# Optimization experiments

Measured on AMD Instinct MI355X. Metric: run time of the kernel, lower is better.

The kernel has to match this reference:

```python
import jax, jax.numpy as jnp
import numpy as np

DIM = 1024
NUM_HEADS = 16
HEAD_DIM = DIM // NUM_HEADS


def setup_inputs() -> dict:
    key = jax.random.key(0)
    ks = jax.random.split(key, 9)
    B, T, D = 4, 8192, DIM
    s = 1.0 / np.sqrt(D)
    return {
        "x": jax.random.normal(ks[0], (B, T, D), dtype=jnp.float32),
        "Wq": jax.random.normal(ks[1], (D, D), dtype=jnp.float32) * s,
        "bq": jnp.zeros((D,), dtype=jnp.float32),
        "Wk": jax.random.normal(ks[2], (D, D), dtype=jnp.float32) * s,
        "bk": jnp.zeros((D,), dtype=jnp.float32),
        "Wv": jax.random.normal(ks[3], (D, D), dtype=jnp.float32) * s,
        "bv": jnp.zeros((D,), dtype=jnp.float32),
        "Wo": jax.random.normal(ks[4], (D, D), dtype=jnp.float32) * s,
        "bo": jnp.zeros((D,), dtype=jnp.float32),
    }


def _feature_map(x):
    # elu(x) + 1
    return jax.nn.elu(x) + 1.0


def reference(x, Wq, bq, Wk, bk, Wv, bv, Wo, bo):
    B, T, D = x.shape
    H, hd = NUM_HEADS, HEAD_DIM
    q = (x @ Wq.T + bq).reshape(B, T, H, hd)
    k = (x @ Wk.T + bk).reshape(B, T, H, hd)
    v = (x @ Wv.T + bv).reshape(B, T, H, hd)
    q = _feature_map(q)
    k = _feature_map(k)
    eps = 1e-6
    kv = jnp.einsum('bthd,bthm->bhmd', k, v)      # [B,H,hd,hd]
    k_sum = k.sum(axis=1)                          # [B,H,hd]
    z = 1.0 / (jnp.einsum('bthd,bhd->bth', q, k_sum) + eps)
    out = jnp.einsum('bthd,bhmd->bthm', q, kv) * z[..., None]
    out = out.reshape(B, T, D)
    return out @ Wo.T + bo
```

## Files before the change

### kernel.cpp

```cpp
#include <hip/hip_runtime.h>
#include <stdint.h>

typedef __bf16 bf16x8 __attribute__((ext_vector_type(8)));
typedef float f32x4 __attribute__((ext_vector_type(4)));
typedef unsigned short u16x8 __attribute__((ext_vector_type(8)));
typedef unsigned short u16x4 __attribute__((ext_vector_type(4)));

#define MFMA16(a, b, c) __builtin_amdgcn_mfma_f32_16x16x32_bf16(a, b, c, 0, 0, 0)
#define BAR() __builtin_amdgcn_s_barrier()
#define LGK0() do { asm volatile("s_waitcnt lgkmcnt(0)" ::: "memory"); \
                    __builtin_amdgcn_sched_barrier(0); } while (0)
#define VMC(n) asm volatile("s_waitcnt vmcnt(" #n ")" ::: "memory")
#define PRIO(p) __builtin_amdgcn_s_setprio(p)

#define TSEQ 8192
#define BATCH 4

static __device__ __forceinline__ unsigned short f2bf(float f) {
  union { float f; unsigned u; } v; v.f = f;
  unsigned u = v.u + 0x7FFFu + ((v.u >> 16) & 1u);
  return (unsigned short)(u >> 16);
}
static __device__ __forceinline__ float bf2f(unsigned short h) {
  union { unsigned u; float f; } v; v.u = ((unsigned)h) << 16; return v.f;
}
static __device__ __forceinline__ void gload16(const void* g, void* l) {
  __builtin_amdgcn_global_load_lds((const __attribute__((address_space(1))) void*)g,
                                   (__attribute__((address_space(3))) void*)l, 16, 0, 0);
}

__global__ __launch_bounds__(256) void cvt_bf16(const float* __restrict__ s,
                                                unsigned short* __restrict__ d, int n) {
  int i = (blockIdx.x * 256 + threadIdx.x) * 8;
  if (i >= n) return;
  const float4 a = *(const float4*)(s + i);
  const float4 b = *(const float4*)(s + i + 4);
  u16x8 o;
  o[0] = f2bf(a.x); o[1] = f2bf(a.y); o[2] = f2bf(a.z); o[3] = f2bf(a.w);
  o[4] = f2bf(b.x); o[5] = f2bf(b.y); o[6] = f2bf(b.z); o[7] = f2bf(b.w);
  *(u16x8*)(d + i) = o;
}


static __device__ __forceinline__ void stage_ht(const unsigned short* __restrict__ G,
                                                int grow0, char* Lbase, int t, int h,
                                                int tid, int w) {
  const int prow = tid >> 2, cp = tid & 3;
  const int gch = cp ^ ((prow >> 1) & 3);
  const unsigned short* src = G + (size_t)(grow0 + h * 128 + prow) * 1024 + t * 32 + gch * 8;
  char* dst = Lbase + (t & 1) * 16384 + h * 8192 + w * 1024;
  gload16(src, dst);
}

static __device__ __forceinline__ void mfma_quad(f32x4 acc[8][4], const bf16x8* a,
                                                 const bf16x8* b, int m0) {
  #pragma unroll
  for (int mf = 0; mf < 4; ++mf)
    #pragma unroll
    for (int nf = 0; nf < 4; ++nf)
      acc[m0 + mf][nf] = MFMA16(a[m0 + mf], b[nf], acc[m0 + mf][nf]);
}

static __device__ __forceinline__ void gemm256(const unsigned short* __restrict__ A,
                                               const unsigned short* __restrict__ B,
                                               int rowA0, int rowB0,
                                               char* As, char* Bs, f32x4 acc[8][4]) {
  const int tid = threadIdx.x, l = tid & 63, w = tid >> 6;
  const int wr = w >> 2, wc = w & 3;
  int a_off[8], b_off[4];
  #pragma unroll
  for (int mf = 0; mf < 8; ++mf) {
    const int r = wr * 128 + mf * 16 + (l & 15);
    const int cp = (l >> 4) ^ ((r >> 1) & 3);
    a_off[mf] = r * 64 + cp * 16;
  }
  #pragma unroll
  for (int nf = 0; nf < 4; ++nf) {
    const int r = wc * 64 + nf * 16 + (l & 15);
    const int cp = (l >> 4) ^ ((r >> 1) & 3);
    b_off[nf] = r * 64 + cp * 16;
  }
  stage_ht(A, rowA0, As, 0, 0, tid, w);
  stage_ht(A, rowA0, As, 0, 1, tid, w);
  stage_ht(B, rowB0, Bs, 0, 0, tid, w);
  stage_ht(B, rowB0, Bs, 0, 1, tid, w);
  stage_ht(A, rowA0, As, 1, 0, tid, w);
  stage_ht(A, rowA0, As, 1, 1, tid, w);
  VMC(2);
  BAR();

  #pragma unroll 1
  for (int i = 0; i < 15; ++i) {
    const int t1 = 2 * i + 1;
    bf16x8 a0[8], b0[4];
    #pragma unroll
    for (int mf = 0; mf < 8; ++mf) a0[mf] = *(const bf16x8*)(As + a_off[mf]);
    #pragma unroll
    for (int nf = 0; nf < 4; ++nf) b0[nf] = *(const bf16x8*)(Bs + b_off[nf]);
    stage_ht(B, rowB0, Bs, t1, 0, tid, w);
    stage_ht(B, rowB0, Bs, t1, 1, tid, w);
    BAR(); LGK0(); PRIO(1);
    mfma_quad(acc, a0, b0, 0);
    PRIO(0); BAR();
    stage_ht(A, rowA0, As, t1 + 1, 0, tid, w);
    stage_ht(A, rowA0, As, t1 + 1, 1, tid, w);
    BAR(); PRIO(1);
    mfma_quad(acc, a0, b0, 4);
    PRIO(0);
    VMC(2);
    BAR();
    bf16x8 a1[8], b1[4];
    #pragma unroll
    for (int mf = 0; mf < 8; ++mf) a1[mf] = *(const bf16x8*)(As + 16384 + a_off[mf]);
    #pragma unroll
    for (int nf = 0; nf < 4; ++nf) b1[nf] = *(const bf16x8*)(Bs + 16384 + b_off[nf]);
    stage_ht(B, rowB0, Bs, t1 + 1, 0, tid, w);
    stage_ht(B, rowB0, Bs, t1 + 1, 1, tid, w);
    BAR(); LGK0(); PRIO(1);
    mfma_quad(acc, a1, b1, 0);
    PRIO(0); BAR();
    stage_ht(A, rowA0, As, t1 + 2, 0, tid, w);
    stage_ht(A, rowA0, As, t1 + 2, 1, tid, w);
    BAR(); PRIO(1);
    mfma_quad(acc, a1, b1, 4);
    PRIO(0);
    VMC(2);
    BAR();
  }
  {
    bf16x8 a0[8], b0[4];
    #pragma unroll
    for (int mf = 0; mf < 8; ++mf) a0[mf] = *(const bf16x8*)(As + a_off[mf]);
    #pragma unroll
    for (int nf = 0; nf < 4; ++nf) b0[nf] = *(const bf16x8*)(Bs + b_off[nf]);
    stage_ht(B, rowB0, Bs, 31, 0, tid, w);
    stage_ht(B, rowB0, Bs, 31, 1, tid, w);
    BAR(); LGK0(); PRIO(1);
    mfma_quad(acc, a0, b0, 0);
    PRIO(0); BAR();
    PRIO(1);
    mfma_quad(acc, a0, b0, 4);
    PRIO(0);
    VMC(0);
    BAR();
    bf16x8 a1[8], b1[4];
    #pragma unroll
    for (int mf = 0; mf < 8; ++mf) a1[mf] = *(const bf16x8*)(As + 16384 + a_off[mf]);
    #pragma unroll
    for (int nf = 0; nf < 4; ++nf) b1[nf] = *(const bf16x8*)(Bs + 16384 + b_off[nf]);
    LGK0(); PRIO(1);
    mfma_quad(acc, a1, b1, 0);
    mfma_quad(acc, a1, b1, 4);
    PRIO(0);
  }
}

__global__ __launch_bounds__(512, 2) void qkv_gemm256(
    const unsigned short* __restrict__ xbf, const unsigned short* __restrict__ wcat,
    const float* __restrict__ bq, const float* __restrict__ bk, const float* __restrict__ bv,
    unsigned short* __restrict__ qout, unsigned short* __restrict__ kout,
    unsigned short* __restrict__ vout) {
  __shared__ char As[32768];
  __shared__ char Bs[32768];
  const int swz = (blockIdx.x & 7) * 192 + (blockIdx.x >> 3);
  const int mt = swz / 12, nt = swz % 12;
  f32x4 acc[8][4] = {};
  gemm256(xbf, wcat, mt * 256, nt * 256, As, Bs, acc);

  const int l = threadIdx.x & 63, w = threadIdx.x >> 6;
  const int wr = w >> 2, wc = w & 3;
  const int region = nt >> 2;
  const float* bias = (region == 0) ? bq : (region == 1) ? bk : bv;
  unsigned short* dst = (region == 0) ? qout : (region == 1) ? kout : vout;
  const int colb = (nt & 3) * 256 + wc * 64;
  #pragma unroll
  for (int mf = 0; mf < 8; ++mf) {
    #pragma unroll
    for (int nf = 0; nf < 4; ++nf) {
      const int col = colb + nf * 16 + (l & 15);
      const float bb = bias[col];
      #pragma unroll
      for (int j = 0; j < 4; ++j) {
        const int row = mt * 256 + wr * 128 + mf * 16 + (l >> 4) * 4 + j;
        float v = acc[mf][nf][j] + bb;
        if (region < 2) v = (v > 0.f) ? (v + 1.f) : __expf(v);
        dst[(size_t)row * 1024 + col] = f2bf(v);
      }
    }
  }
}

__global__ __launch_bounds__(512, 2) void o_gemm256(
    const unsigned short* __restrict__ attn, const unsigned short* __restrict__ wo,
    const float* __restrict__ bo, float* __restrict__ out) {
  __shared__ char As[32768];
  __shared__ char Bs[32768];
  const int swz = (blockIdx.x & 7) * 64 + (blockIdx.x >> 3);
  const int mt = swz >> 2, nt = swz & 3;
  f32x4 acc[8][4] = {};
  gemm256(attn, wo, mt * 256, nt * 256, As, Bs, acc);

  const int l = threadIdx.x & 63, w = threadIdx.x >> 6;
  const int wr = w >> 2, wc = w & 3;
  #pragma unroll
  for (int mf = 0; mf < 8; ++mf) {
    #pragma unroll
    for (int nf = 0; nf < 4; ++nf) {
      const int col = nt * 256 + wc * 64 + nf * 16 + (l & 15);
      const float bb = bo[col];
      #pragma unroll
      for (int j = 0; j < 4; ++j) {
        const int row = mt * 256 + wr * 128 + mf * 16 + (l >> 4) * 4 + j;
        out[(size_t)row * 1024 + col] = acc[mf][nf][j] + bb;
      }
    }
  }
}

__global__ __launch_bounds__(64) void kv_reduce(const unsigned short* __restrict__ kbf,
                                                const unsigned short* __restrict__ vbf,
                                                float* __restrict__ part) {
  const int bh = blockIdx.x, tc = blockIdx.y;
  const int b = bh >> 4, h = bh & 15;
  const int l = threadIdx.x;
  const int tm = l & 15, td = l >> 4;
  const unsigned short* kb = kbf + (size_t)b * TSEQ * 1024 + h * 64;
  const unsigned short* vb = vbf + (size_t)b * TSEQ * 1024 + h * 64;
  float acc[4][16] = {};
  float ksum = 0.f;
  const int t0 = tc * 256;
  #pragma unroll 2
  for (int t = t0; t < t0 + 256; ++t) {
    const unsigned short* krow = kb + (size_t)t * 1024;
    const unsigned short* vrow = vb + (size_t)t * 1024;
    const u16x8 k8a = *(const u16x8*)(krow + td * 16);
    const u16x8 k8b = *(const u16x8*)(krow + td * 16 + 8);
    const u16x4 v4 = *(const u16x4*)(vrow + tm * 4);
    float kf[16];
    #pragma unroll
    for (int j = 0; j < 8; ++j) { kf[j] = bf2f(k8a[j]); kf[8 + j] = bf2f(k8b[j]); }
    float vf[4];
    #pragma unroll
    for (int i = 0; i < 4; ++i) vf[i] = bf2f(v4[i]);
    ksum += bf2f(krow[td * 16 + tm]);
    #pragma unroll
    for (int i = 0; i < 4; ++i)
      #pragma unroll
      for (int j = 0; j < 16; ++j)
        acc[i][j] += vf[i] * kf[j];
  }
  float* ps = part + (size_t)(tc * 64 + bh) * 65 * 64;
  #pragma unroll
  for (int i = 0; i < 4; ++i) {
    const int m = tm * 4 + i;
    #pragma unroll
    for (int j = 0; j < 16; j += 4) {
      float4 o = make_float4(acc[i][j], acc[i][j + 1], acc[i][j + 2], acc[i][j + 3]);
      *(float4*)(ps + m * 64 + td * 16 + j) = o;
    }
  }
  ps[64 * 64 + td * 16 + tm] = ksum;
}

__global__ __launch_bounds__(256) void kv_finalize(const float* __restrict__ part,
                                                   unsigned short* __restrict__ bmat) {
  const int e = blockIdx.x * 256 + threadIdx.x;
  if (e >= 64 * 80 * 64) return;
  const int d = e & 63;
  const int r = (e >> 6) % 80;
  const int bh = e / (80 * 64);
  float s = 0.f;
  if (r < 65) {
    #pragma unroll
    for (int tc = 0; tc < 32; ++tc)
      s += part[((size_t)(tc * 64 + bh) * 65 + r) * 64 + d];
  }
  bmat[e] = f2bf(s);
}

__global__ __launch_bounds__(256) void attn_gemm(const unsigned short* __restrict__ qbf,
                                                 const unsigned short* __restrict__ bmat,
                                                 unsigned short* __restrict__ attn) {
  __shared__ char Qs[16384];
  __shared__ char Bs2[10240];
  const int bh = blockIdx.x, mt = blockIdx.y;
  const int b = bh >> 4, h = bh & 15;
  const int tid = threadIdx.x, l = tid & 63, w = tid >> 6;

  const unsigned short* qbase = qbf + (size_t)(b * TSEQ + mt * 128) * 1024 + h * 64;
  #pragma unroll
  for (int r4 = 0; r4 < 4; ++r4) {
    const int ci = r4 * 256 + tid;
    const int row = ci >> 3;
    const int csrc = (ci & 7) ^ (row & 7);
    gload16(qbase + (size_t)row * 1024 + csrc * 8, Qs + (r4 * 256 + w * 64) * 16);
  }
  const unsigned short* bbase = bmat + (size_t)bh * 80 * 64;
  #pragma unroll
  for (int r4 = 0; r4 < 3; ++r4) {
    const int ci = r4 * 256 + tid;
    if (ci < 640) {
      const int row = ci >> 3;
      const int csrc = (ci & 7) ^ (row & 7);
      gload16(bbase + row * 64 + csrc * 8, Bs2 + (r4 * 256 + w * 64) * 16);
    }
  }
  __syncthreads();

  f32x4 acc[2][5] = {};
  #pragma unroll
  for (int ks = 0; ks < 2; ++ks) {
    bf16x8 af[2], bfr[5];
    #pragma unroll
    for (int m = 0; m < 2; ++m) {
      const int r = w * 32 + m * 16 + (l & 15);
      const int c = ((l >> 4) + ks * 4) ^ (r & 7);
      af[m] = *(const bf16x8*)(Qs + r * 128 + c * 16);
    }
    #pragma unroll
    for (int n = 0; n < 5; ++n) {
      const int r = n * 16 + (l & 15);
      const int c = ((l >> 4) + ks * 4) ^ (r & 7);
      bfr[n] = *(const bf16x8*)(Bs2 + r * 128 + c * 16);
    }
    #pragma unroll
    for (int m = 0; m < 2; ++m)
      #pragma unroll
      for (int n = 0; n < 5; ++n)
        acc[m][n] = MFMA16(af[m], bfr[n], acc[m][n]);
  }

  unsigned short* arow = attn + (size_t)(b * TSEQ + mt * 128) * 1024 + h * 64;
  #pragma unroll
  for (int m = 0; m < 2; ++m) {
    #pragma unroll
    for (int j = 0; j < 4; ++j) {
      const float den = __shfl(acc[m][4][j], (l & 48));
      const float z = 1.f / (den + 1e-6f);
      const int row = w * 32 + m * 16 + (l >> 4) * 4 + j;
      #pragma unroll
      for (int n = 0; n < 4; ++n)
        arow[(size_t)row * 1024 + n * 16 + (l & 15)] = f2bf(acc[m][n][j] * z);
    }
  }
}

extern "C" void kernel_launch(void* const* d_in, const int* in_sizes, int n_in,
                              void* d_out, int out_size, void* d_ws, size_t ws_size,
                              hipStream_t stream) {
  const float* x  = (const float*)d_in[0];
  const float* Wq = (const float*)d_in[1];
  const float* bq = (const float*)d_in[2];
  const float* Wk = (const float*)d_in[3];
  const float* bk = (const float*)d_in[4];
  const float* Wv = (const float*)d_in[5];
  const float* bv = (const float*)d_in[6];
  const float* Wo = (const float*)d_in[7];
  const float* bo = (const float*)d_in[8];
  float* out = (float*)d_out;
  char* ws = (char*)d_ws;

  unsigned short* xbf  = (unsigned short*)(ws + 0);
  unsigned short* wcat = (unsigned short*)(ws + 67108864);
  unsigned short* wobf = (unsigned short*)(ws + 73400320);
  unsigned short* qbf  = (unsigned short*)(ws + 75497472);
  unsigned short* kbf  = (unsigned short*)(ws + 142606336);
  unsigned short* vbf  = (unsigned short*)(ws + 209715200);
  float* part          = (float*)(ws + 0);
  unsigned short* bmat = (unsigned short*)(ws + 34078720);
  unsigned short* attn = kbf;

  cvt_bf16<<<16384, 256, 0, stream>>>(x, xbf, 33554432);
  cvt_bf16<<<512, 256, 0, stream>>>(Wq, wcat, 1048576);
  cvt_bf16<<<512, 256, 0, stream>>>(Wk, wcat + 1048576, 1048576);
  cvt_bf16<<<512, 256, 0, stream>>>(Wv, wcat + 2097152, 1048576);
  cvt_bf16<<<512, 256, 0, stream>>>(Wo, wobf, 1048576);

  qkv_gemm256<<<1536, 512, 0, stream>>>(xbf, wcat, bq, bk, bv, qbf, kbf, vbf);
  kv_reduce<<<dim3(64, 32), 64, 0, stream>>>(kbf, vbf, part);
  kv_finalize<<<1280, 256, 0, stream>>>(part, bmat);
  attn_gemm<<<dim3(64, 64), 256, 0, stream>>>(qbf, bmat, attn);
  o_gemm256<<<512, 512, 0, stream>>>(attn, wobf, bo, out);
}
```

Before: 699.1 us.

## Restructure 256x256 GEMM mainloop with 64-wide K tiles and quadrant pipelining

The shared GEMM mainloop for the QKV and output projections now stages 64-wide K tiles into 128 KB of double-buffered LDS instead of 32-wide tiles. Each tile is computed in four MFMA quadrants, with LDS fragment loads and global prefetches interleaved between them under a new XOR swizzle. This is meant to halve the number of barrier-heavy K iterations and hide more load latency behind MFMA work. In exchange, the LDS footprint per block rises to 128 KB, which likely limits occupancy to one block per CU despite the launch bound of 2. The four weight-conversion launches are also merged into one kernel.

```diff
diff --git a/kernel.cpp b/kernel.cpp
--- a/kernel.cpp
+++ b/kernel.cpp
@@ -41,24 +41,108 @@
   *(u16x8*)(d + i) = o;
 }
 
-
-static __device__ __forceinline__ void stage_ht(const unsigned short* __restrict__ G,
-                                                int grow0, char* Lbase, int t, int h,
-                                                int tid, int w) {
-  const int prow = tid >> 2, cp = tid & 3;
-  const int gch = cp ^ ((prow >> 1) & 3);
-  const unsigned short* src = G + (size_t)(grow0 + h * 128 + prow) * 1024 + t * 32 + gch * 8;
-  char* dst = Lbase + (t & 1) * 16384 + h * 8192 + w * 1024;
-  gload16(src, dst);
-}
-
-static __device__ __forceinline__ void mfma_quad(f32x4 acc[8][4], const bf16x8* a,
-                                                 const bf16x8* b, int m0) {
-  #pragma unroll
-  for (int mf = 0; mf < 4; ++mf)
-    #pragma unroll
-    for (int nf = 0; nf < 4; ++nf)
-      acc[m0 + mf][nf] = MFMA16(a[m0 + mf], b[nf], acc[m0 + mf][nf]);
+__global__ __launch_bounds__(256) void cvt_weights(const float* __restrict__ wq,
+                                                   const float* __restrict__ wk,
+                                                   const float* __restrict__ wv,
+                                                   const float* __restrict__ wo,
+                                                   unsigned short* __restrict__ wcat,
+                                                   unsigned short* __restrict__ wobf) {
+  const int r = blockIdx.x >> 9;
+  const float* s = (r == 0) ? wq : (r == 1) ? wk : (r == 2) ? wv : wo;
+  unsigned short* d = (r < 3) ? (wcat + r * 1048576) : wobf;
+  const int i = ((blockIdx.x & 511) * 256 + threadIdx.x) * 8;
+  const float4 a = *(const float4*)(s + i);
+  const float4 b = *(const float4*)(s + i + 4);
+  u16x8 o;
+  o[0] = f2bf(a.x); o[1] = f2bf(a.y); o[2] = f2bf(a.z); o[3] = f2bf(a.w);
+  o[4] = f2bf(b.x); o[5] = f2bf(b.y); o[6] = f2bf(b.z); o[7] = f2bf(b.w);
+  *(u16x8*)(d + i) = o;
+}
+
+
+static __device__ __forceinline__ void stage_half(const unsigned short* __restrict__ G,
+                                                  int grow0, char* L, int t, int h,
+                                                  int tid, int w) {
+  #pragma unroll
+  for (int j = 0; j < 2; ++j) {
+    const int ci = j * 512 + tid;
+    const int rr = ci >> 3;
+    const int gch = (ci & 7) ^ (rr & 7);
+    gload16(G + (size_t)(grow0 + h * 128 + rr) * 1024 + t * 64 + gch * 8,
+            L + (t & 1) * 32768 + h * 16384 + j * 8192 + w * 1024);
+  }
+}
+
+template <bool S1, bool S3, bool S4, int VM>
+static __device__ __forceinline__ void tile_body(
+    const unsigned short* __restrict__ A, const unsigned short* __restrict__ B,
+    int rowA0, int rowB0, char* As, char* Bs, int t, f32x4 acc[8][4],
+    int Abase, int Bbase, int tid, int w) {
+  const int buf = (t & 1) * 32768;
+  bf16x8 a0[4][2], a1[4][2], b0[2][2], b1[2][2];
+  #pragma unroll
+  for (int mf = 0; mf < 4; ++mf)
+    #pragma unroll
+    for (int ks = 0; ks < 2; ++ks)
+      a0[mf][ks] = *(const bf16x8*)(As + ((buf + Abase + mf * 2048) ^ (ks << 6)));
+  #pragma unroll
+  for (int nf = 0; nf < 2; ++nf)
+    #pragma unroll
+    for (int ks = 0; ks < 2; ++ks)
+      b0[nf][ks] = *(const bf16x8*)(Bs + ((buf + Bbase + nf * 2048) ^ (ks << 6)));
+  if (S1) stage_half(A, rowA0, As, t + 1, 1, tid, w);
+  BAR(); LGK0(); PRIO(1);
+  #pragma unroll
+  for (int mf = 0; mf < 4; ++mf)
+    #pragma unroll
+    for (int nf = 0; nf < 2; ++nf)
+      #pragma unroll
+      for (int ks = 0; ks < 2; ++ks)
+        acc[mf][nf] = MFMA16(a0[mf][ks], b0[nf][ks], acc[mf][nf]);
+  PRIO(0); BAR();
+  #pragma unroll
+  for (int nf = 0; nf < 2; ++nf)
+    #pragma unroll
+    for (int ks = 0; ks < 2; ++ks)
+      b1[nf][ks] = *(const bf16x8*)(Bs + ((buf + Bbase + (nf + 2) * 2048) ^ (ks << 6)));
+  BAR(); LGK0(); PRIO(1);
+  #pragma unroll
+  for (int mf = 0; mf < 4; ++mf)
+    #pragma unroll
+    for (int nf = 0; nf < 2; ++nf)
+      #pragma unroll
+      for (int ks = 0; ks < 2; ++ks)
+        acc[mf][nf + 2] = MFMA16(a0[mf][ks], b1[nf][ks], acc[mf][nf + 2]);
+  PRIO(0); BAR();
+  #pragma unroll
+  for (int mf = 0; mf < 4; ++mf)
+    #pragma unroll
+    for (int ks = 0; ks < 2; ++ks)
+      a1[mf][ks] = *(const bf16x8*)(As + ((buf + Abase + (mf + 4) * 2048) ^ (ks << 6)));
+  if (S3) {
+    stage_half(B, rowB0, Bs, t + 2, 0, tid, w);
+    stage_half(B, rowB0, Bs, t + 2, 1, tid, w);
+  }
+  BAR(); LGK0(); PRIO(1);
+  #pragma unroll
+  for (int mf = 0; mf < 4; ++mf)
+    #pragma unroll
+    for (int nf = 0; nf < 2; ++nf)
+      #pragma unroll
+      for (int ks = 0; ks < 2; ++ks)
+        acc[mf + 4][nf + 2] = MFMA16(a1[mf][ks], b1[nf][ks], acc[mf + 4][nf + 2]);
+  PRIO(0); BAR();
+  if (S4) stage_half(A, rowA0, As, t + 2, 0, tid, w);
+  if (VM == 6) { VMC(6); } else { VMC(0); }
+  BAR(); PRIO(1);
+  #pragma unroll
+  for (int mf = 0; mf < 4; ++mf)
+    #pragma unroll
+    for (int nf = 0; nf < 2; ++nf)
+      #pragma unroll
+      for (int ks = 0; ks < 2; ++ks)
+        acc[mf + 4][nf] = MFMA16(a1[mf][ks], b0[nf][ks], acc[mf + 4][nf]);
+  PRIO(0); BAR();
 }
 
 static __device__ __forceinline__ void gemm256(const unsigned short* __restrict__ A,
@@ -67,92 +151,22 @@
                                                char* As, char* Bs, f32x4 acc[8][4]) {
   const int tid = threadIdx.x, l = tid & 63, w = tid >> 6;
   const int wr = w >> 2, wc = w & 3;
-  int a_off[8], b_off[4];
-  #pragma unroll
-  for (int mf = 0; mf < 8; ++mf) {
-    const int r = wr * 128 + mf * 16 + (l & 15);
-    const int cp = (l >> 4) ^ ((r >> 1) & 3);
-    a_off[mf] = r * 64 + cp * 16;
-  }
-  #pragma unroll
-  for (int nf = 0; nf < 4; ++nf) {
-    const int r = wc * 64 + nf * 16 + (l & 15);
-    const int cp = (l >> 4) ^ ((r >> 1) & 3);
-    b_off[nf] = r * 64 + cp * 16;
-  }
-  stage_ht(A, rowA0, As, 0, 0, tid, w);
-  stage_ht(A, rowA0, As, 0, 1, tid, w);
-  stage_ht(B, rowB0, Bs, 0, 0, tid, w);
-  stage_ht(B, rowB0, Bs, 0, 1, tid, w);
-  stage_ht(A, rowA0, As, 1, 0, tid, w);
-  stage_ht(A, rowA0, As, 1, 1, tid, w);
-  VMC(2);
-  BAR();
-
+  const int cp0 = (l >> 4) ^ (l & 7);
+  const int Abase = (wr * 128 + (l & 15)) * 128 + cp0 * 16;
+  const int Bbase = (wc * 64 + (l & 15)) * 128 + cp0 * 16;
+  stage_half(A, rowA0, As, 0, 0, tid, w);
+  stage_half(A, rowA0, As, 0, 1, tid, w);
+  stage_half(B, rowB0, Bs, 0, 0, tid, w);
+  stage_half(B, rowB0, Bs, 0, 1, tid, w);
+  stage_half(B, rowB0, Bs, 1, 0, tid, w);
+  stage_half(B, rowB0, Bs, 1, 1, tid, w);
+  stage_half(A, rowA0, As, 1, 0, tid, w);
+  VMC(6); BAR();
   #pragma unroll 1
-  for (int i = 0; i < 15; ++i) {
-    const int t1 = 2 * i + 1;
-    bf16x8 a0[8], b0[4];
-    #pragma unroll
-    for (int mf = 0; mf < 8; ++mf) a0[mf] = *(const bf16x8*)(As + a_off[mf]);
-    #pragma unroll
-    for (int nf = 0; nf < 4; ++nf) b0[nf] = *(const bf16x8*)(Bs + b_off[nf]);
-    stage_ht(B, rowB0, Bs, t1, 0, tid, w);
-    stage_ht(B, rowB0, Bs, t1, 1, tid, w);
-    BAR(); LGK0(); PRIO(1);
-    mfma_quad(acc, a0, b0, 0);
-    PRIO(0); BAR();
-    stage_ht(A, rowA0, As, t1 + 1, 0, tid, w);
-    stage_ht(A, rowA0, As, t1 + 1, 1, tid, w);
-    BAR(); PRIO(1);
-    mfma_quad(acc, a0, b0, 4);
-    PRIO(0);
-    VMC(2);
-    BAR();
-    bf16x8 a1[8], b1[4];
-    #pragma unroll
-    for (int mf = 0; mf < 8; ++mf) a1[mf] = *(const bf16x8*)(As + 16384 + a_off[mf]);
-    #pragma unroll
-    for (int nf = 0; nf < 4; ++nf) b1[nf] = *(const bf16x8*)(Bs + 16384 + b_off[nf]);
-    stage_ht(B, rowB0, Bs, t1 + 1, 0, tid, w);
-    stage_ht(B, rowB0, Bs, t1 + 1, 1, tid, w);
-    BAR(); LGK0(); PRIO(1);
-    mfma_quad(acc, a1, b1, 0);
-    PRIO(0); BAR();
-    stage_ht(A, rowA0, As, t1 + 2, 0, tid, w);
-    stage_ht(A, rowA0, As, t1 + 2, 1, tid, w);
-    BAR(); PRIO(1);
-    mfma_quad(acc, a1, b1, 4);
-    PRIO(0);
-    VMC(2);
-    BAR();
-  }
-  {
-    bf16x8 a0[8], b0[4];
-    #pragma unroll
-    for (int mf = 0; mf < 8; ++mf) a0[mf] = *(const bf16x8*)(As + a_off[mf]);
-    #pragma unroll
-    for (int nf = 0; nf < 4; ++nf) b0[nf] = *(const bf16x8*)(Bs + b_off[nf]);
-    stage_ht(B, rowB0, Bs, 31, 0, tid, w);
-    stage_ht(B, rowB0, Bs, 31, 1, tid, w);
-    BAR(); LGK0(); PRIO(1);
-    mfma_quad(acc, a0, b0, 0);
-    PRIO(0); BAR();
-    PRIO(1);
-    mfma_quad(acc, a0, b0, 4);
-    PRIO(0);
-    VMC(0);
-    BAR();
-    bf16x8 a1[8], b1[4];
-    #pragma unroll
-    for (int mf = 0; mf < 8; ++mf) a1[mf] = *(const bf16x8*)(As + 16384 + a_off[mf]);
-    #pragma unroll
-    for (int nf = 0; nf < 4; ++nf) b1[nf] = *(const bf16x8*)(Bs + 16384 + b_off[nf]);
-    LGK0(); PRIO(1);
-    mfma_quad(acc, a1, b1, 0);
-    mfma_quad(acc, a1, b1, 4);
-    PRIO(0);
-  }
+  for (int t = 0; t < 14; ++t)
+    tile_body<true, true, true, 6>(A, B, rowA0, rowB0, As, Bs, t, acc, Abase, Bbase, tid, w);
+  tile_body<true, false, false, 0>(A, B, rowA0, rowB0, As, Bs, 14, acc, Abase, Bbase, tid, w);
+  tile_body<false, false, false, 0>(A, B, rowA0, rowB0, As, Bs, 15, acc, Abase, Bbase, tid, w);
 }
 
 __global__ __launch_bounds__(512, 2) void qkv_gemm256(
@@ -160,8 +174,9 @@
     const float* __restrict__ bq, const float* __restrict__ bk, const float* __restrict__ bv,
     unsigned short* __restrict__ qout, unsigned short* __restrict__ kout,
     unsigned short* __restrict__ vout) {
-  __shared__ char As[32768];
-  __shared__ char Bs[32768];
+  __shared__ char smem[131072];
+  char* As = smem;
+  char* Bs = smem + 65536;
   const int swz = (blockIdx.x & 7) * 192 + (blockIdx.x >> 3);
   const int mt = swz / 12, nt = swz % 12;
   f32x4 acc[8][4] = {};
@@ -193,8 +208,9 @@
 __global__ __launch_bounds__(512, 2) void o_gemm256(
     const unsigned short* __restrict__ attn, const unsigned short* __restrict__ wo,
     const float* __restrict__ bo, float* __restrict__ out) {
-  __shared__ char As[32768];
-  __shared__ char Bs[32768];
+  __shared__ char smem[131072];
+  char* As = smem;
+  char* Bs = smem + 65536;
   const int swz = (blockIdx.x & 7) * 64 + (blockIdx.x >> 3);
   const int mt = swz >> 2, nt = swz & 3;
   f32x4 acc[8][4] = {};
@@ -371,10 +387,7 @@
   unsigned short* attn = kbf;
 
   cvt_bf16<<<16384, 256, 0, stream>>>(x, xbf, 33554432);
-  cvt_bf16<<<512, 256, 0, stream>>>(Wq, wcat, 1048576);
-  cvt_bf16<<<512, 256, 0, stream>>>(Wk, wcat + 1048576, 1048576);
-  cvt_bf16<<<512, 256, 0, stream>>>(Wv, wcat + 2097152, 1048576);
-  cvt_bf16<<<512, 256, 0, stream>>>(Wo, wobf, 1048576);
+  cvt_weights<<<2048, 256, 0, stream>>>(Wq, Wk, Wv, Wo, wcat, wobf);
 
   qkv_gemm256<<<1536, 512, 0, stream>>>(xbf, wcat, bq, bk, bv, qbf, kbf, vbf);
   kv_reduce<<<dim3(64, 32), 64, 0, stream>>>(kbf, vbf, part);
```

Measured after the change: 674.3 us. -3.6%, faster.
